# Optimization experiments

Hardware: AMD Instinct MI355X
Metric: run time of the kernel (lower is better)

## Reference

```python
import jax, jax.numpy as jnp
import numpy as np

B, T, L, H, P = 256, 2048, 4, 64, 1  # batch, seq_len, layers, hidden_size, proj_size(=input_size)


def setup_inputs() -> dict:
    key = jax.random.key(0)
    ks = jax.random.split(key, 6)
    s = 0.1  # keep recurrent dynamics stable
    return {
        "y": jax.random.normal(ks[0], (B, T, P), jnp.float32),
        "W_ih": jax.random.normal(ks[1], (L, 4 * H, P), jnp.float32) * s,
        "W_hh": jax.random.normal(ks[2], (L, 4 * H, P), jnp.float32) * s,
        "b_ih": jax.random.normal(ks[3], (L, 4 * H), jnp.float32) * s,
        "b_hh": jax.random.normal(ks[4], (L, 4 * H), jnp.float32) * s,
        "W_hr": jax.random.normal(ks[5], (L, P, H), jnp.float32) * s,
        "min_seq_len": 1,
    }


def _lstm_layer(x, wih, whh, bih, bhh, whr):
    # x: [B, T, in]; torch gate order: i, f, g, o. proj_size: h = W_hr @ (o * tanh(c)).
    Bq = x.shape[0]
    hid = whh.shape[0] // 4
    gx = jnp.einsum('bti,gi->btg', x, wih) + bih + bhh  # [B, T, 4H], input GEMM batched over time
    h0 = jnp.zeros((Bq, whr.shape[0]), x.dtype)  # projected hidden [B, P]
    c0 = jnp.zeros((Bq, hid), x.dtype)           # cell [B, H]

    def step(carry, g_t):
        h, c = carry
        g = g_t + h @ whh.T  # [B, 4H]
        i, f, gg, o = jnp.split(g, 4, axis=-1)
        c = jax.nn.sigmoid(f) * c + jax.nn.sigmoid(i) * jnp.tanh(gg)
        h = (jax.nn.sigmoid(o) * jnp.tanh(c)) @ whr.T  # project H -> P
        return (h, c), h

    _, hs = jax.lax.scan(step, (h0, c0), jnp.swapaxes(gx, 0, 1))  # time-major scan
    return jnp.swapaxes(hs, 0, 1)  # [B, T, P]


def reference(y, W_ih, W_hh, b_ih, b_hh, W_hr, min_seq_len):
    x = y
    for l in range(W_ih.shape[0]):  # static layer loop (4 layers)
        x = _lstm_layer(x, W_ih[l], W_hh[l], b_ih[l], b_hh[l], W_hr[l])
    return x[:, min_seq_len:]  # matches self.layer(y)[0][:, min_seq_len:]
```

## Files before the change

### kernel.cpp

```cpp
#include <hip/hip_runtime.h>

#define BATCH  256
#define SEQT   2048
#define LAYERS 4
#define CHUNK  32
#define HALF   16
#define PHASES (SEQT / CHUNK + LAYERS - 1)

#define LOG2E  1.4426950408889634f
#define K2     (2.0f * LOG2E)
#define HID    64

__device__ __forceinline__ float fast_rcp(float x) {
    return __builtin_amdgcn_rcpf(x);
}
__device__ __forceinline__ float fast_exp2(float x) {
    return __builtin_amdgcn_exp2f(x);
}

#define DPP_ADD(v, ctrl)                                                     \
    (v) += __int_as_float(__builtin_amdgcn_update_dpp(                       \
        0, __float_as_int(v), (ctrl), 0xF, 0xF, true))

__device__ __forceinline__ float wave_sum_lane63(float v) {
    DPP_ADD(v, 0x111);
    DPP_ADD(v, 0x112);
    DPP_ADD(v, 0x114);
    DPP_ADD(v, 0x118);
    DPP_ADD(v, 0x142);
    DPP_ADD(v, 0x143);
    return v;
}

__global__ __launch_bounds__(256, 1) void lstm_pipeline_kernel(
    const float* __restrict__ y,
    const float* __restrict__ W_ih,
    const float* __restrict__ W_hh,
    const float* __restrict__ b_ih,
    const float* __restrict__ b_hh,
    const float* __restrict__ W_hr,
    const int*  __restrict__ msl_p,
    float* __restrict__ out)
{
    const int b   = blockIdx.x;
    const int tid = threadIdx.x;
    const int l   = tid >> 6;
    const int k   = tid & 63;
    const int msl = *msl_p;

    __shared__ float y_lds[SEQT];
    __shared__ float out_lds[SEQT];
    __shared__ __align__(16) float h_buf[2][LAYERS][CHUNK];

    {
        const float4* y4  = (const float4*)(y + (size_t)b * SEQT);
        float4*       yl4 = (float4*)y_lds;
        #pragma unroll
        for (int i = tid; i < SEQT / 4; i += 256) yl4[i] = y4[i];
    }

    const int wbase = l * 4 * HID;
    const float wi0 = -LOG2E * W_ih[wbase + 0 * HID + k];
    const float wi1 = -LOG2E * W_ih[wbase + 1 * HID + k];
    const float wi2 =  K2    * W_ih[wbase + 2 * HID + k];
    const float wi3 = -LOG2E * W_ih[wbase + 3 * HID + k];
    const float wh0 = -LOG2E * W_hh[wbase + 0 * HID + k];
    const float wh1 = -LOG2E * W_hh[wbase + 1 * HID + k];
    const float wh2 =  K2    * W_hh[wbase + 2 * HID + k];
    const float wh3 = -LOG2E * W_hh[wbase + 3 * HID + k];
    const float bb0 = -LOG2E * (b_ih[wbase + 0 * HID + k] + b_hh[wbase + 0 * HID + k]);
    const float bb1 = -LOG2E * (b_ih[wbase + 1 * HID + k] + b_hh[wbase + 1 * HID + k]);
    const float bb2 =  K2    * (b_ih[wbase + 2 * HID + k] + b_hh[wbase + 2 * HID + k]);
    const float bb3 = -LOG2E * (b_ih[wbase + 3 * HID + k] + b_hh[wbase + 3 * HID + k]);
    const float wr  = W_hr[l * HID + k];

    float h = 0.0f;
    float C = 0.0f;

    for (int p = 0; p < PHASES; ++p) {
        __syncthreads();
        const int t0 = (p - l) * CHUNK;
        if (t0 >= 0 && t0 < SEQT) {
            float4 xv[CHUNK / 4];
            if (l == 0) {
                const float4* ys = (const float4*)&y_lds[t0];
                #pragma unroll
                for (int q = 0; q < CHUNK / 4; ++q) xv[q] = ys[q];
            } else {
                const float4* hb = (const float4*)&h_buf[(p - 1) & 1][l - 1][0];
                #pragma unroll
                for (int q = 0; q < CHUNK / 4; ++q) xv[q] = hb[q];
            }
            float xs[CHUNK];
            #pragma unroll
            for (int q = 0; q < CHUNK / 4; ++q) {
                xs[4 * q + 0] = xv[q].x; xs[4 * q + 1] = xv[q].y;
                xs[4 * q + 2] = xv[q].z; xs[4 * q + 3] = xv[q].w;
            }

            float hcol = 0.0f;

            #pragma unroll
            for (int half = 0; half < CHUNK / HALF; ++half) {
                const int jb = half * HALF;

                float p0[HALF], p1[HALF], p2[HALF], p3[HALF];
                #pragma unroll
                for (int j = 0; j < HALF; ++j) {
                    const float x = xs[jb + j];
                    p0[j] = fmaf(x, wi0, bb0);
                    p1[j] = fmaf(x, wi1, bb1);
                    p2[j] = fmaf(x, wi2, bb2);
                    p3[j] = fmaf(x, wi3, bb3);
                }

                #pragma unroll
                for (int j = 0; j < HALF; ++j) {
                    const float gi = fmaf(h, wh0, p0[j]);
                    const float gf = fmaf(h, wh1, p1[j]);
                    const float gg = fmaf(h, wh2, p2[j]);
                    const float go = fmaf(h, wh3, p3[j]);

                    const float Ei = fast_exp2(gi);
                    const float Ef = fast_exp2(gf);
                    const float Eg = fast_exp2(gg);
                    const float Eo = fast_exp2(go);

                    const float ai     = 1.0f + Ei;
                    const float ag     = 1.0f + Eg;
                    const float af     = 1.0f + Ef;
                    const float den_ig = ai * ag;
                    const float tg     = fmaf(K2, Eg, -K2);
                    const float tgf    = tg * af;
                    const float num    = fmaf(C, den_ig, tgf);
                    const float den    = den_ig * af;
                    C = num * fast_rcp(den);

                    const float Ec   = fast_exp2(C);
                    const float ao   = 1.0f + Eo;
                    const float ac   = 1.0f + Ec;
                    const float den2 = ao * ac;
                    const float num2 = fmaf(wr, Ec, -wr);
                    const float v    = num2 * fast_rcp(den2);

                    const float vs = wave_sum_lane63(v);

                    h = __int_as_float(
                        __builtin_amdgcn_readlane(__float_as_int(vs), 63));

                    hcol = (k == jb + j) ? h : hcol;
                }
            }

            if (k < CHUNK) {
                if (l < LAYERS - 1) h_buf[p & 1][l][k] = hcol;
                else                out_lds[t0 + k]    = hcol;
            }
        }
    }

    __syncthreads();
    const int nout = SEQT - msl;
    float* outb = out + (size_t)b * nout;
    for (int i = tid; i < nout; i += 256) outb[i] = out_lds[i + msl];
}

extern "C" void kernel_launch(void* const* d_in, const int* in_sizes, int n_in,
                              void* d_out, int out_size, void* d_ws, size_t ws_size,
                              hipStream_t stream) {
    const float* y    = (const float*)d_in[0];
    const float* W_ih = (const float*)d_in[1];
    const float* W_hh = (const float*)d_in[2];
    const float* b_ih = (const float*)d_in[3];
    const float* b_hh = (const float*)d_in[4];
    const float* W_hr = (const float*)d_in[5];
    const int*   msl  = (const int*)d_in[6];
    float* out = (float*)d_out;

    lstm_pipeline_kernel<<<BATCH, 256, 0, stream>>>(
        y, W_ih, W_hh, b_ih, b_hh, W_hr, msl, out);
}
```

Measured before the change: 313.4 us.

## Replace per-phase block barriers with LDS flag-based producer/consumer wave pipeline

Drops the per-phase __syncthreads lockstep between layer waves. Each layer wave now spin-waits on an LDS flag written by the previous layer, and inter-layer outputs go into full-length LDS buffers instead of a double buffer. Layers can run decoupled, so a slow wave no longer stalls the others at every chunk, and the ramp-up and ramp-down phases where waves sat idle at the barrier go away. The trade-offs are spin-wait polling with s_sleep, extra LDS use, and reliance on memory fences being correct for wave-to-wave signalling.

Result: faster. 297.9 us (median of 2 runs) (-5.0%).

```diff
diff --git a/kernel.cpp b/kernel.cpp
--- a/kernel.cpp
+++ b/kernel.cpp
@@ -5,11 +5,11 @@
 #define LAYERS 4
 #define CHUNK  32
 #define HALF   16
-#define PHASES (SEQT / CHUNK + LAYERS - 1)
+#define NCHUNK (SEQT / CHUNK)
+#define HID    64
 
 #define LOG2E  1.4426950408889634f
 #define K2     (2.0f * LOG2E)
-#define HID    64
 
 __device__ __forceinline__ float fast_rcp(float x) {
     return __builtin_amdgcn_rcpf(x);
@@ -49,14 +49,16 @@
     const int msl = *msl_p;
 
     __shared__ float y_lds[SEQT];
+    __shared__ float inter[LAYERS - 1][SEQT];
     __shared__ float out_lds[SEQT];
-    __shared__ __align__(16) float h_buf[2][LAYERS][CHUNK];
+    __shared__ int   flags[LAYERS];
 
     {
         const float4* y4  = (const float4*)(y + (size_t)b * SEQT);
         float4*       yl4 = (float4*)y_lds;
         #pragma unroll
         for (int i = tid; i < SEQT / 4; i += 256) yl4[i] = y4[i];
+        if (tid < LAYERS) flags[tid] = 0;
     }
 
     const int wbase = l * 4 * HID;
@@ -74,88 +76,95 @@
     const float bb3 = -LOG2E * (b_ih[wbase + 3 * HID + k] + b_hh[wbase + 3 * HID + k]);
     const float wr  = W_hr[l * HID + k];
 
+    __syncthreads();
+
     float h = 0.0f;
     float C = 0.0f;
 
-    for (int p = 0; p < PHASES; ++p) {
-        __syncthreads();
-        const int t0 = (p - l) * CHUNK;
-        if (t0 >= 0 && t0 < SEQT) {
-            float4 xv[CHUNK / 4];
-            if (l == 0) {
-                const float4* ys = (const float4*)&y_lds[t0];
-                #pragma unroll
-                for (int q = 0; q < CHUNK / 4; ++q) xv[q] = ys[q];
-            } else {
-                const float4* hb = (const float4*)&h_buf[(p - 1) & 1][l - 1][0];
-                #pragma unroll
-                for (int q = 0; q < CHUNK / 4; ++q) xv[q] = hb[q];
-            }
-            float xs[CHUNK];
+    volatile int* vflags = flags;
+
+    for (int c = 0; c < NCHUNK; ++c) {
+        const int t0 = c * CHUNK;
+
+        if (l > 0) {
+            while (vflags[l - 1] <= c) __builtin_amdgcn_s_sleep(1);
+            __threadfence_block();
+        }
+
+        const float* src = (l == 0) ? &y_lds[t0] : &inter[l - 1][t0];
+        float4 xv[CHUNK / 4];
+        {
+            const float4* s4 = (const float4*)src;
             #pragma unroll
-            for (int q = 0; q < CHUNK / 4; ++q) {
-                xs[4 * q + 0] = xv[q].x; xs[4 * q + 1] = xv[q].y;
-                xs[4 * q + 2] = xv[q].z; xs[4 * q + 3] = xv[q].w;
+            for (int q = 0; q < CHUNK / 4; ++q) xv[q] = s4[q];
+        }
+        float xs[CHUNK];
+        #pragma unroll
+        for (int q = 0; q < CHUNK / 4; ++q) {
+            xs[4 * q + 0] = xv[q].x; xs[4 * q + 1] = xv[q].y;
+            xs[4 * q + 2] = xv[q].z; xs[4 * q + 3] = xv[q].w;
+        }
+
+        float hcol = 0.0f;
+
+        #pragma unroll
+        for (int half = 0; half < CHUNK / HALF; ++half) {
+            const int jb = half * HALF;
+
+            float p0[HALF], p1[HALF], p2[HALF], p3[HALF];
+            #pragma unroll
+            for (int j = 0; j < HALF; ++j) {
+                const float x = xs[jb + j];
+                p0[j] = fmaf(x, wi0, bb0);
+                p1[j] = fmaf(x, wi1, bb1);
+                p2[j] = fmaf(x, wi2, bb2);
+                p3[j] = fmaf(x, wi3, bb3);
             }
 
-            float hcol = 0.0f;
+            #pragma unroll
+            for (int j = 0; j < HALF; ++j) {
+                const float gi = fmaf(h, wh0, p0[j]);
+                const float gf = fmaf(h, wh1, p1[j]);
+                const float gg = fmaf(h, wh2, p2[j]);
+                const float go = fmaf(h, wh3, p3[j]);
 
-            #pragma unroll
-            for (int half = 0; half < CHUNK / HALF; ++half) {
-                const int jb = half * HALF;
+                const float Ei = fast_exp2(gi);
+                const float Ef = fast_exp2(gf);
+                const float Eg = fast_exp2(gg);
+                const float Eo = fast_exp2(go);
 
-                float p0[HALF], p1[HALF], p2[HALF], p3[HALF];
-                #pragma unroll
-                for (int j = 0; j < HALF; ++j) {
-                    const float x = xs[jb + j];
-                    p0[j] = fmaf(x, wi0, bb0);
-                    p1[j] = fmaf(x, wi1, bb1);
-                    p2[j] = fmaf(x, wi2, bb2);
-                    p3[j] = fmaf(x, wi3, bb3);
-                }
+                const float ai     = 1.0f + Ei;
+                const float ag     = 1.0f + Eg;
+                const float af     = 1.0f + Ef;
+                const float den_ig = ai * ag;
+                const float tg     = fmaf(K2, Eg, -K2);
+                const float tgf    = tg * af;
+                const float num    = fmaf(C, den_ig, tgf);
+                const float den    = den_ig * af;
+                C = num * fast_rcp(den);
 
-                #pragma unroll
-                for (int j = 0; j < HALF; ++j) {
-                    const float gi = fmaf(h, wh0, p0[j]);
-                    const float gf = fmaf(h, wh1, p1[j]);
-                    const float gg = fmaf(h, wh2, p2[j]);
-                    const float go = fmaf(h, wh3, p3[j]);
+                const float Ec   = fast_exp2(C);
+                const float ao   = 1.0f + Eo;
+                const float ac   = 1.0f + Ec;
+                const float den2 = ao * ac;
+                const float num2 = fmaf(wr, Ec, -wr);
+                const float v    = num2 * fast_rcp(den2);
 
-                    const float Ei = fast_exp2(gi);
-                    const float Ef = fast_exp2(gf);
-                    const float Eg = fast_exp2(gg);
-                    const float Eo = fast_exp2(go);
+                const float vs = wave_sum_lane63(v);
 
-                    const float ai     = 1.0f + Ei;
-                    const float ag     = 1.0f + Eg;
-                    const float af     = 1.0f + Ef;
-                    const float den_ig = ai * ag;
-                    const float tg     = fmaf(K2, Eg, -K2);
-                    const float tgf    = tg * af;
-                    const float num    = fmaf(C, den_ig, tgf);
-                    const float den    = den_ig * af;
-                    C = num * fast_rcp(den);
+                h = __int_as_float(
+                    __builtin_amdgcn_readlane(__float_as_int(vs), 63));
 
-                    const float Ec   = fast_exp2(C);
-                    const float ao   = 1.0f + Eo;
-                    const float ac   = 1.0f + Ec;
-                    const float den2 = ao * ac;
-                    const float num2 = fmaf(wr, Ec, -wr);
-                    const float v    = num2 * fast_rcp(den2);
+                hcol = (k == jb + j) ? h : hcol;
+            }
+        }
 
-                    const float vs = wave_sum_lane63(v);
-
-                    h = __int_as_float(
-                        __builtin_amdgcn_readlane(__float_as_int(vs), 63));
-
-                    hcol = (k == jb + j) ? h : hcol;
-                }
-            }
-
-            if (k < CHUNK) {
-                if (l < LAYERS - 1) h_buf[p & 1][l][k] = hcol;
-                else                out_lds[t0 + k]    = hcol;
-            }
+        if (l < LAYERS - 1) {
+            if (k < CHUNK) inter[l][t0 + k] = hcol;
+            __threadfence_block();
+            if (k == 0) vflags[l] = c + 1;
+        } else {
+            if (k < CHUNK) out_lds[t0 + k] = hcol;
         }
     }
 
```
